# Kernel optimization log

Measured on AMD Instinct MI355X. Metric: run time of the kernel, lower is better.

The kernel has to match this reference:

```python
import jax, jax.numpy as jnp
import numpy as np


def psf2otf(psf, shape):
    """Zero-pad psf to `shape` and circularly shift so its center is at the
    origin, then 2D FFT. psf: [..., kh, kw] -> complex [..., H, W]."""
    kh, kw = psf.shape[-2], psf.shape[-1]
    H, W = shape
    pad = jnp.zeros(psf.shape[:-2] + (H, W), psf.dtype)
    pad = pad.at[..., :kh, :kw].set(psf)
    pad = jnp.roll(pad, shift=(-(kh // 2), -(kw // 2)), axis=(-2, -1))
    return jnp.fft.fft2(pad)


def setup_inputs() -> dict:
    key = jax.random.key(0)
    k1, k2, k3, k4, k5 = jax.random.split(key, 5)
    B, C, H, W = 4, 3, 512, 512
    NF, FS, KS = 24, 5, 25
    y = jax.random.normal(k1, (B, C, H, W), dtype=jnp.float32)
    k = jax.random.uniform(k2, (B, 1, KS, KS), dtype=jnp.float32)
    k = k / jnp.sum(k, axis=(-2, -1), keepdims=True)  # normalized blur PSF
    w = 0.5 + jax.random.uniform(k3, (B, 1), dtype=jnp.float32)  # positive (Softplus output)
    phi = jax.random.normal(k4, (B, C, H, W), dtype=jnp.float32)
    weights = jax.random.normal(k5, (NF, C, FS, FS), dtype=jnp.float32) * 0.3
    return {"y": y, "k": k, "w": w, "phi": phi, "weights": weights}


def reference(y, k, w, phi, weights):
    # FFT-domain Wiener deconvolution (FourierDeconvolutionFunction_init.forward).
    B, C, H, W = y.shape
    Fy = jnp.fft.fft2(y)                         # [B,C,H,W] complex64
    Dg = psf2otf(weights, (H, W))                # [NF,C,H,W] complex64
    Dk = psf2otf(k, (H, W))                      # [B,1,H,W] complex64, broadcasts over C
    w4 = w[:, :, None, None]                     # [B,1,1,1]
    Fphi = jnp.fft.fft2(phi / w4)                # [B,C,H,W]
    Dg_sum = jnp.sum(jnp.abs(Dg) ** 2, axis=0)[None] / w4   # [B,C,H,W] real
    Omega = 1.0 / (jnp.abs(Dk) ** 2 + Dg_sum)    # [B,C,H,W] real
    num = Omega * (jnp.conj(Dk) * Fy + Fphi)     # [B,C,H,W] complex64
    out = jnp.real(jnp.fft.ifft2(num)).astype(y.dtype)  # torch.irfft(..., onesided=False)
    return out
```

## Files before the change

### kernel.cpp

```cpp
#include <hip/hip_runtime.h>
#include <math.h>

#define PI_F 3.14159265358979323846f
#define NPIX 262144

__device__ __forceinline__ float2 cmul(float2 a, float2 b) {
    return make_float2(a.x * b.x - a.y * b.y, a.x * b.y + a.y * b.x);
}
__device__ __forceinline__ float2 cadd(float2 a, float2 b) {
    return make_float2(a.x + b.x, a.y + b.y);
}
__device__ __forceinline__ float2 csub(float2 a, float2 b) {
    return make_float2(a.x - b.x, a.y - b.y);
}

template<int DIR>
__device__ __forceinline__ void fill_tw(float2* tw, int t) {
    for (int m = t; m < 384; m += 128) {
        float s, c;
        sincosf((float)DIR * (2.0f * PI_F) * (float)m * (1.0f / 512.0f), &s, &c);
        tw[m] = make_float2(c, s);
    }
}

template<int DIR>
__device__ __forceinline__ float2* fft512(float2* sA, float2* sB,
                                          const float2* tw, int t) {
    float2* X = sA;
    float2* Y = sB;
    int Ns = 1;
#pragma unroll
    for (int s = 0; s < 4; ++s) {
        const int jm = t & (Ns - 1);
        const int jd = t - jm;
        float2 v0 = X[t], v1 = X[t + 128], v2 = X[t + 256], v3 = X[t + 384];
        const int m1 = jm * (128 / Ns);
        v1 = cmul(tw[m1], v1);
        v2 = cmul(tw[2 * m1], v2);
        v3 = cmul(tw[3 * m1], v3);
        const float2 t0 = cadd(v0, v2), t1 = csub(v0, v2);
        const float2 t2 = cadd(v1, v3), t3 = csub(v1, v3);
        const float2 t3i = (DIR > 0) ? make_float2(-t3.y, t3.x)
                                     : make_float2(t3.y, -t3.x);
        const int od = (jd << 2) + jm;
        Y[od]          = cadd(t0, t2);
        Y[od + Ns]     = cadd(t1, t3i);
        Y[od + 2 * Ns] = csub(t0, t2);
        Y[od + 3 * Ns] = csub(t1, t3i);
        __syncthreads();
        float2* tmp = X; X = Y; Y = tmp;
        Ns <<= 2;
    }
#pragma unroll
    for (int q = 0; q < 2; ++q) {
        const int j = t + q * 128;
        const float2 a = X[j], b = X[j + 256];
        const float2 tt = cmul(tw[j], b);
        Y[j]       = cadd(a, tt);
        Y[j + 256] = csub(a, tt);
    }
    __syncthreads();
    return Y;
}

__global__ __launch_bounds__(128) void fwd_fft_pack(const float* __restrict__ y,
                                                    const float* __restrict__ phi,
                                                    const float* __restrict__ w,
                                                    float2* __restrict__ S) {
    __shared__ float2 sA[512], sB[512], tw[384];
    const int t = threadIdx.x;
    const int img = blockIdx.x >> 9, row = blockIdx.x & 511;
    fill_tw<-1>(tw, t);
    const size_t off = (size_t)img * NPIX + (size_t)row * 512;
    const float iwv = 1.0f / w[img / 3];
    const float4 yv = ((const float4*)(y + off))[t];
    const float4 pv = ((const float4*)(phi + off))[t];
    sA[4 * t + 0] = make_float2(yv.x, pv.x * iwv);
    sA[4 * t + 1] = make_float2(yv.y, pv.y * iwv);
    sA[4 * t + 2] = make_float2(yv.z, pv.z * iwv);
    sA[4 * t + 3] = make_float2(yv.w, pv.w * iwv);
    __syncthreads();
    float2* R = fft512<-1>(sA, sB, tw, t);
    float4* wp = (float4*)(S + off);
    for (int k = t; k < 256; k += 128)
        wp[k] = make_float4(R[2 * k].x, R[2 * k].y,
                            R[2 * k + 1].x, R[2 * k + 1].y);
}

__global__ __launch_bounds__(128) void fwd_fft_kg(float2* __restrict__ S) {
    __shared__ float2 sA[512], sB[512], tw[384];
    const int t = threadIdx.x;
    int img, row;
    if (blockIdx.x < 100) {
        img = 12 + (int)blockIdx.x / 25;
        row = ((int)blockIdx.x % 25 - 12) & 511;
    } else {
        const int g = (int)blockIdx.x - 100;
        img = 16 + g / 9;
        row = ((g % 9) - 4) & 511;
    }
    fill_tw<-1>(tw, t);
    float2* rp = S + (size_t)img * NPIX + (size_t)row * 512;
    for (int k = t; k < 512; k += 128) sA[k] = rp[k];
    __syncthreads();
    float2* R = fft512<-1>(sA, sB, tw, t);
    for (int k = t; k < 512; k += 128) rp[k] = R[k];
}

template<int DIR>
__global__ __launch_bounds__(128) void fft_rows(float2* __restrict__ D) {
    __shared__ float2 sA[512], sB[512], tw[384];
    const int t = threadIdx.x;
    fill_tw<DIR>(tw, t);
    float2* rp = D + (size_t)blockIdx.x * 512;
    const float4* rp4 = (const float4*)rp;
    for (int k = t; k < 256; k += 128) {
        const float4 v = rp4[k];
        sA[2 * k]     = make_float2(v.x, v.y);
        sA[2 * k + 1] = make_float2(v.z, v.w);
    }
    __syncthreads();
    float2* R = fft512<DIR>(sA, sB, tw, t);
    float4* wp = (float4*)rp;
    for (int k = t; k < 256; k += 128)
        wp[k] = make_float4(R[2 * k].x, R[2 * k].y,
                            R[2 * k + 1].x, R[2 * k + 1].y);
}

__global__ __launch_bounds__(128) void inv_fft_unpack(const float2* __restrict__ T,
                                                      float* __restrict__ out) {
    __shared__ float2 sA[512], sB[512], tw[384];
    const int t = threadIdx.x;
    const int pair = blockIdx.x >> 9, row = blockIdx.x & 511;
    fill_tw<1>(tw, t);
    const float2* rp = T + (size_t)pair * NPIX + (size_t)row * 512;
    const float4* rp4 = (const float4*)rp;
    for (int k = t; k < 256; k += 128) {
        const float4 v = rp4[k];
        sA[2 * k]     = make_float2(v.x, v.y);
        sA[2 * k + 1] = make_float2(v.z, v.w);
    }
    __syncthreads();
    float2* R = fft512<1>(sA, sB, tw, t);
    const float sc = 1.0f / 262144.0f;
    float* o0 = out + (size_t)(2 * pair) * NPIX + (size_t)row * 512;
    float* o1 = o0 + NPIX;
    ((float4*)o0)[t] = make_float4(R[4 * t].x * sc, R[4 * t + 1].x * sc,
                                   R[4 * t + 2].x * sc, R[4 * t + 3].x * sc);
    ((float4*)o1)[t] = make_float4(R[4 * t].y * sc, R[4 * t + 1].y * sc,
                                   R[4 * t + 2].y * sc, R[4 * t + 3].y * sc);
}

__global__ __launch_bounds__(256) void transpose512_inplace(float2* __restrict__ D) {
    if (blockIdx.x > blockIdx.y) return;
    __shared__ float2 tA[32][33], tB[32][33];
    const size_t base = (size_t)blockIdx.z * NPIX;
    const int bi = blockIdx.x * 32, bj = blockIdx.y * 32;
    const int tx = threadIdx.x, ty = threadIdx.y;
    const bool diag = (bi == bj);
#pragma unroll
    for (int j = 0; j < 32; j += 8)
        tA[ty + j][tx] = D[base + (size_t)(bj + ty + j) * 512 + bi + tx];
    if (!diag) {
#pragma unroll
        for (int j = 0; j < 32; j += 8)
            tB[ty + j][tx] = D[base + (size_t)(bi + ty + j) * 512 + bj + tx];
    }
    __syncthreads();
#pragma unroll
    for (int j = 0; j < 32; j += 8)
        D[base + (size_t)(bi + ty + j) * 512 + bj + tx] = tA[tx][ty + j];
    if (!diag) {
#pragma unroll
        for (int j = 0; j < 32; j += 8)
            D[base + (size_t)(bj + ty + j) * 512 + bi + tx] = tB[tx][ty + j];
    }
}

__global__ __launch_bounds__(256) void transpose512(const float2* __restrict__ in,
                                                    float2* __restrict__ out) {
    __shared__ float2 tile[32][33];
    const size_t base = (size_t)blockIdx.z * NPIX;
    const int bx = blockIdx.x * 32, by = blockIdx.y * 32;
    const int tx = threadIdx.x, ty = threadIdx.y;
#pragma unroll
    for (int j = 0; j < 32; j += 8)
        tile[ty + j][tx] = in[base + (size_t)(by + ty + j) * 512 + bx + tx];
    __syncthreads();
#pragma unroll
    for (int j = 0; j < 32; j += 8)
        out[base + (size_t)(bx + ty + j) * 512 + by + tx] = tile[tx][ty + j];
}

__global__ __launch_bounds__(256) void prep_kg(const float* __restrict__ kin,
                                               const float* __restrict__ wts,
                                               float2* __restrict__ S) {
    const int bid = blockIdx.x, tid = threadIdx.x;
    if (bid < 10) {
        const int t = bid * 256 + tid;
        if (t < 2500) {
            const int b = t / 625, rem = t % 625;
            const int i = rem / 25, j = rem % 25;
            const int r = (i - 12) & 511, c = (j - 12) & 511;
            S[(size_t)(12 + b) * NPIX + (size_t)r * 512 + c] =
                make_float2(kin[t], 0.0f);
        }
        return;
    }
    const int ch = bid - 10;
    __shared__ float gp[24][13][13];
    __shared__ float part[243];
    float* gpf = &gp[0][0][0];
    for (int i = tid; i < 24 * 169; i += 256) gpf[i] = 0.0f;
    __syncthreads();
    for (int i = tid; i < 600; i += 256) {
        const int f = i / 25, rem = i % 25;
        const int x = rem / 5, yy = rem % 5;
        gp[f][x + 4][yy + 4] = wts[(size_t)(f * 3 + ch) * 25 + rem];
    }
    __syncthreads();
    if (tid < 243) {
        const int dpos = tid / 3, seg = tid % 3;
        const int di = dpos / 9 - 4, dj = dpos % 9 - 4;
        float acc = 0.0f;
        for (int f = seg * 8; f < seg * 8 + 8; ++f) {
#pragma unroll
            for (int x = 0; x < 5; ++x)
#pragma unroll
                for (int yy = 0; yy < 5; ++yy)
                    acc += gp[f][x + 4][yy + 4] *
                           gp[f][x + di + 4][yy + dj + 4];
        }
        part[tid] = acc;
    }
    __syncthreads();
    if (tid < 81) {
        const float a = part[tid * 3] + part[tid * 3 + 1] + part[tid * 3 + 2];
        const int di = tid / 9 - 4, dj = tid % 9 - 4;
        const int r = di & 511, c = dj & 511;
        S[(size_t)(16 + ch) * NPIX + (size_t)r * 512 + c] =
            make_float2(a, 0.0f);
    }
}

__global__ __launch_bounds__(256) void combine_pack(const float2* __restrict__ S,
                                                    const float* __restrict__ w,
                                                    float2* __restrict__ P) {
    const int p = blockIdx.x * 256 + threadIdx.x;
    const int pair = blockIdx.y;
    const int r = p >> 9, c = p & 511;
    const int np = (((512 - r) & 511) << 9) | ((512 - c) & 511);
    float2 num[2];
#pragma unroll
    for (int e = 0; e < 2; ++e) {
        const int img = pair * 2 + e;
        const int b = img / 3;
        const int ch = img - 3 * b;
        const float2* Zi = S + (size_t)img * NPIX;
        const float2 Zv = Zi[p];
        const float2 Zn = Zi[np];
        const float2 Zm = make_float2(Zn.x, -Zn.y);
        const float2 Fy = make_float2(0.5f * (Zv.x + Zm.x),
                                      0.5f * (Zv.y + Zm.y));
        const float dx = Zv.x - Zm.x, dy = Zv.y - Zm.y;
        const float2 Fphi = make_float2(0.5f * dy, -0.5f * dx);
        const float2 K = S[(size_t)(12 + b) * NPIX + p];
        const float kk = K.x * K.x + K.y * K.y;
        const float dg = S[(size_t)(16 + ch) * NPIX + p].x / w[b];
        const float Om = 1.0f / (kk + dg);
        const float2 tt = make_float2(K.x * Fy.x + K.y * Fy.y,
                                      K.x * Fy.y - K.y * Fy.x);
        num[e] = make_float2(Om * (tt.x + Fphi.x), Om * (tt.y + Fphi.y));
    }
    P[(size_t)pair * NPIX + p] =
        make_float2(num[0].x - num[1].y, num[0].y + num[1].x);
}

extern "C" void kernel_launch(void* const* d_in, const int* in_sizes, int n_in,
                              void* d_out, int out_size, void* d_ws, size_t ws_size,
                              hipStream_t stream) {
    const float* y   = (const float*)d_in[0];
    const float* k   = (const float*)d_in[1];
    const float* w   = (const float*)d_in[2];
    const float* phi = (const float*)d_in[3];
    const float* wts = (const float*)d_in[4];
    float* out = (float*)d_out;

    const size_t needed = (size_t)25 * NPIX * sizeof(float2);
    if (ws_size < needed) return;
    float2* S = (float2*)d_ws;
    float2* P = S + (size_t)19 * NPIX;

    hipMemsetAsync(S + (size_t)12 * NPIX, 0,
                   (size_t)7 * NPIX * sizeof(float2), stream);

    prep_kg<<<13, 256, 0, stream>>>(k, wts, S);
    fwd_fft_pack<<<12 * 512, 128, 0, stream>>>(y, phi, w, S);
    fwd_fft_kg<<<127, 128, 0, stream>>>(S);

    dim3 tb(32, 8);
    transpose512_inplace<<<dim3(16, 16, 19), tb, 0, stream>>>(S);
    fft_rows<-1><<<19 * 512, 128, 0, stream>>>(S);

    combine_pack<<<dim3(1024, 6), 256, 0, stream>>>(S, w, P);

    fft_rows<1><<<6 * 512, 128, 0, stream>>>(P);
    transpose512<<<dim3(16, 16, 6), tb, 0, stream>>>(P, S);
    inv_fft_unpack<<<6 * 512, 128, 0, stream>>>(S, out);
}
```

Measured before the change: 164.9 us.

## Fuse spectral combine into first inverse FFT pass and merge forward FFT launches

The pointwise Wiener combine is fused into the first inverse row-FFT pass. Each block handles a row and its mirror row, so the conjugate-symmetric partner data is read from the same pair of rows and the intermediate P array is never written and re-read by a separate kernel. The two forward FFT launches (image rows and the kernel/filter rows) are merged into one grid, which saves a launch. Twiddles now use the fast __sinf/__cosf intrinsics, trading some accuracy for cheaper setup.

```diff
diff --git a/kernel.cpp b/kernel.cpp
--- a/kernel.cpp
+++ b/kernel.cpp
@@ -15,11 +15,11 @@
 }
 
 template<int DIR>
-__device__ __forceinline__ void fill_tw(float2* tw, int t) {
-    for (int m = t; m < 384; m += 128) {
-        float s, c;
-        sincosf((float)DIR * (2.0f * PI_F) * (float)m * (1.0f / 512.0f), &s, &c);
-        tw[m] = make_float2(c, s);
+__device__ __forceinline__ void fill_tw(float2* tw, int t, int stride) {
+    for (int m = t; m < 384; m += stride) {
+        const float ang = (2.0f * PI_F / 512.0f) * (float)m;
+        const float s = __sinf(ang), c = __cosf(ang);
+        tw[m] = make_float2(c, (DIR > 0) ? s : -s);
     }
 }
 
@@ -63,43 +63,41 @@
     return Y;
 }
 
-__global__ __launch_bounds__(128) void fwd_fft_pack(const float* __restrict__ y,
-                                                    const float* __restrict__ phi,
-                                                    const float* __restrict__ w,
-                                                    float2* __restrict__ S) {
+__global__ __launch_bounds__(128) void fwd_fft_all(const float* __restrict__ y,
+                                                   const float* __restrict__ phi,
+                                                   const float* __restrict__ w,
+                                                   float2* __restrict__ S) {
     __shared__ float2 sA[512], sB[512], tw[384];
     const int t = threadIdx.x;
-    const int img = blockIdx.x >> 9, row = blockIdx.x & 511;
-    fill_tw<-1>(tw, t);
-    const size_t off = (size_t)img * NPIX + (size_t)row * 512;
-    const float iwv = 1.0f / w[img / 3];
-    const float4 yv = ((const float4*)(y + off))[t];
-    const float4 pv = ((const float4*)(phi + off))[t];
-    sA[4 * t + 0] = make_float2(yv.x, pv.x * iwv);
-    sA[4 * t + 1] = make_float2(yv.y, pv.y * iwv);
-    sA[4 * t + 2] = make_float2(yv.z, pv.z * iwv);
-    sA[4 * t + 3] = make_float2(yv.w, pv.w * iwv);
-    __syncthreads();
-    float2* R = fft512<-1>(sA, sB, tw, t);
-    float4* wp = (float4*)(S + off);
-    for (int k = t; k < 256; k += 128)
-        wp[k] = make_float4(R[2 * k].x, R[2 * k].y,
-                            R[2 * k + 1].x, R[2 * k + 1].y);
-}
-
-__global__ __launch_bounds__(128) void fwd_fft_kg(float2* __restrict__ S) {
-    __shared__ float2 sA[512], sB[512], tw[384];
-    const int t = threadIdx.x;
+    fill_tw<-1>(tw, t, 128);
+    if (blockIdx.x < 6144) {
+        const int img = blockIdx.x >> 9, row = blockIdx.x & 511;
+        const size_t off = (size_t)img * NPIX + (size_t)row * 512;
+        const float iwv = 1.0f / w[img / 3];
+        const float4 yv = ((const float4*)(y + off))[t];
+        const float4 pv = ((const float4*)(phi + off))[t];
+        sA[4 * t + 0] = make_float2(yv.x, pv.x * iwv);
+        sA[4 * t + 1] = make_float2(yv.y, pv.y * iwv);
+        sA[4 * t + 2] = make_float2(yv.z, pv.z * iwv);
+        sA[4 * t + 3] = make_float2(yv.w, pv.w * iwv);
+        __syncthreads();
+        float2* R = fft512<-1>(sA, sB, tw, t);
+        float4* wp = (float4*)(S + off);
+        for (int k = t; k < 256; k += 128)
+            wp[k] = make_float4(R[2 * k].x, R[2 * k].y,
+                                R[2 * k + 1].x, R[2 * k + 1].y);
+        return;
+    }
+    const int bid = blockIdx.x - 6144;
     int img, row;
-    if (blockIdx.x < 100) {
-        img = 12 + (int)blockIdx.x / 25;
-        row = ((int)blockIdx.x % 25 - 12) & 511;
+    if (bid < 100) {
+        img = 12 + bid / 25;
+        row = (bid % 25 - 12) & 511;
     } else {
-        const int g = (int)blockIdx.x - 100;
+        const int g = bid - 100;
         img = 16 + g / 9;
         row = ((g % 9) - 4) & 511;
     }
-    fill_tw<-1>(tw, t);
     float2* rp = S + (size_t)img * NPIX + (size_t)row * 512;
     for (int k = t; k < 512; k += 128) sA[k] = rp[k];
     __syncthreads();
@@ -111,7 +109,7 @@
 __global__ __launch_bounds__(128) void fft_rows(float2* __restrict__ D) {
     __shared__ float2 sA[512], sB[512], tw[384];
     const int t = threadIdx.x;
-    fill_tw<DIR>(tw, t);
+    fill_tw<DIR>(tw, t, 128);
     float2* rp = D + (size_t)blockIdx.x * 512;
     const float4* rp4 = (const float4*)rp;
     for (int k = t; k < 256; k += 128) {
@@ -127,12 +125,88 @@
                             R[2 * k + 1].x, R[2 * k + 1].y);
 }
 
+__device__ __forceinline__ float2 get2(const float4 a, const float4 b, int q) {
+    switch (q) {
+        case 0:  return make_float2(a.x, a.y);
+        case 1:  return make_float2(a.z, a.w);
+        case 2:  return make_float2(b.x, b.y);
+        default: return make_float2(b.z, b.w);
+    }
+}
+
+__global__ __launch_bounds__(256) void combine_ifft(const float2* __restrict__ S,
+                                                    const float* __restrict__ w,
+                                                    float2* __restrict__ P) {
+    __shared__ float2 sA[2][512], sB[2][512], tw[384];
+    const int t = threadIdx.x;
+    const int h = t >> 7, tt = t & 127;
+    const int rr = blockIdx.x;
+    const int pair = blockIdx.y;
+    const int r0 = rr, r1 = (512 - rr) & 511;
+    const int rh = h ? r1 : r0;
+    const int ro = h ? r0 : r1;
+    fill_tw<1>(tw, t, 256);
+    const int i0 = 2 * pair, i1 = 2 * pair + 1;
+    const int b0 = i0 / 3, b1 = i1 / 3;
+    const int ch0 = i0 % 3, ch1 = i1 % 3;
+    const float iw0 = 1.0f / w[b0], iw1 = 1.0f / w[b1];
+    const size_t rowh = (size_t)rh * 512, rowo = (size_t)ro * 512;
+    const float4* Zv0 = (const float4*)(S + (size_t)i0 * NPIX + rowh);
+    const float4* Zv1 = (const float4*)(S + (size_t)i1 * NPIX + rowh);
+    const float2* Zn0 = S + (size_t)i0 * NPIX + rowo;
+    const float2* Zn1 = S + (size_t)i1 * NPIX + rowo;
+    const float4* K0 = (const float4*)(S + (size_t)(12 + b0) * NPIX + rowh);
+    const float4* K1 = (const float4*)(S + (size_t)(12 + b1) * NPIX + rowh);
+    const float4* G0 = (const float4*)(S + (size_t)(16 + ch0) * NPIX + rowh);
+    const float4* G1 = (const float4*)(S + (size_t)(16 + ch1) * NPIX + rowh);
+
+    const float4 za = Zv0[2 * tt], zb = Zv0[2 * tt + 1];
+    const float4 ua = Zv1[2 * tt], ub = Zv1[2 * tt + 1];
+    const float4 ka = K0[2 * tt],  kb = K0[2 * tt + 1];
+    const float4 la = K1[2 * tt],  lb = K1[2 * tt + 1];
+    const float4 ga = G0[2 * tt],  gb = G0[2 * tt + 1];
+    const float4 ha = G1[2 * tt],  hb = G1[2 * tt + 1];
+#pragma unroll
+    for (int q = 0; q < 4; ++q) {
+        const int c = 4 * tt + q;
+        const int nc = (512 - c) & 511;
+        float2 num[2];
+#pragma unroll
+        for (int e = 0; e < 2; ++e) {
+            const float2 Zv = e ? get2(ua, ub, q) : get2(za, zb, q);
+            const float2 Zn = e ? Zn1[nc] : Zn0[nc];
+            const float2 K  = e ? get2(la, lb, q) : get2(ka, kb, q);
+            const float dg  = (e ? get2(ha, hb, q).x : get2(ga, gb, q).x) *
+                              (e ? iw1 : iw0);
+            const float2 Zm = make_float2(Zn.x, -Zn.y);
+            const float2 Fy = make_float2(0.5f * (Zv.x + Zm.x),
+                                          0.5f * (Zv.y + Zm.y));
+            const float dx = Zv.x - Zm.x, dy = Zv.y - Zm.y;
+            const float2 Fphi = make_float2(0.5f * dy, -0.5f * dx);
+            const float kk = K.x * K.x + K.y * K.y;
+            const float Om = 1.0f / (kk + dg);
+            const float2 cf = make_float2(K.x * Fy.x + K.y * Fy.y,
+                                          K.x * Fy.y - K.y * Fy.x);
+            num[e] = make_float2(Om * (cf.x + Fphi.x), Om * (cf.y + Fphi.y));
+        }
+        sA[h][c] = make_float2(num[0].x - num[1].y, num[0].y + num[1].x);
+    }
+    __syncthreads();
+    float2* R = fft512<1>(&sA[h][0], &sB[h][0], tw, tt);
+    if (!(h == 1 && r1 == r0)) {
+        float4* wp = (float4*)(P + (size_t)pair * NPIX + rowh);
+        for (int k = tt; k < 256; k += 128)
+            wp[k] = make_float4(R[2 * k].x, R[2 * k].y,
+                                R[2 * k + 1].x, R[2 * k + 1].y);
+    }
+}
+
 __global__ __launch_bounds__(128) void inv_fft_unpack(const float2* __restrict__ T,
                                                       float* __restrict__ out) {
     __shared__ float2 sA[512], sB[512], tw[384];
     const int t = threadIdx.x;
     const int pair = blockIdx.x >> 9, row = blockIdx.x & 511;
-    fill_tw<1>(tw, t);
+    fill_tw<1>(tw, t, 128);
     const float2* rp = T + (size_t)pair * NPIX + (size_t)row * 512;
     const float4* rp4 = (const float4*)rp;
     for (int k = t; k < 256; k += 128) {
@@ -243,39 +317,6 @@
     }
 }
 
-__global__ __launch_bounds__(256) void combine_pack(const float2* __restrict__ S,
-                                                    const float* __restrict__ w,
-                                                    float2* __restrict__ P) {
-    const int p = blockIdx.x * 256 + threadIdx.x;
-    const int pair = blockIdx.y;
-    const int r = p >> 9, c = p & 511;
-    const int np = (((512 - r) & 511) << 9) | ((512 - c) & 511);
-    float2 num[2];
-#pragma unroll
-    for (int e = 0; e < 2; ++e) {
-        const int img = pair * 2 + e;
-        const int b = img / 3;
-        const int ch = img - 3 * b;
-        const float2* Zi = S + (size_t)img * NPIX;
-        const float2 Zv = Zi[p];
-        const float2 Zn = Zi[np];
-        const float2 Zm = make_float2(Zn.x, -Zn.y);
-        const float2 Fy = make_float2(0.5f * (Zv.x + Zm.x),
-                                      0.5f * (Zv.y + Zm.y));
-        const float dx = Zv.x - Zm.x, dy = Zv.y - Zm.y;
-        const float2 Fphi = make_float2(0.5f * dy, -0.5f * dx);
-        const float2 K = S[(size_t)(12 + b) * NPIX + p];
-        const float kk = K.x * K.x + K.y * K.y;
-        const float dg = S[(size_t)(16 + ch) * NPIX + p].x / w[b];
-        const float Om = 1.0f / (kk + dg);
-        const float2 tt = make_float2(K.x * Fy.x + K.y * Fy.y,
-                                      K.x * Fy.y - K.y * Fy.x);
-        num[e] = make_float2(Om * (tt.x + Fphi.x), Om * (tt.y + Fphi.y));
-    }
-    P[(size_t)pair * NPIX + p] =
-        make_float2(num[0].x - num[1].y, num[0].y + num[1].x);
-}
-
 extern "C" void kernel_launch(void* const* d_in, const int* in_sizes, int n_in,
                               void* d_out, int out_size, void* d_ws, size_t ws_size,
                               hipStream_t stream) {
@@ -295,16 +336,14 @@
                    (size_t)7 * NPIX * sizeof(float2), stream);
 
     prep_kg<<<13, 256, 0, stream>>>(k, wts, S);
-    fwd_fft_pack<<<12 * 512, 128, 0, stream>>>(y, phi, w, S);
-    fwd_fft_kg<<<127, 128, 0, stream>>>(S);
+    fwd_fft_all<<<6271, 128, 0, stream>>>(y, phi, w, S);
 
     dim3 tb(32, 8);
     transpose512_inplace<<<dim3(16, 16, 19), tb, 0, stream>>>(S);
     fft_rows<-1><<<19 * 512, 128, 0, stream>>>(S);
 
-    combine_pack<<<dim3(1024, 6), 256, 0, stream>>>(S, w, P);
-
-    fft_rows<1><<<6 * 512, 128, 0, stream>>>(P);
+    combine_ifft<<<dim3(257, 6), 256, 0, stream>>>(S, w, P);
+
     transpose512<<<dim3(16, 16, 6), tb, 0, stream>>>(P, S);
     inv_fft_unpack<<<6 * 512, 128, 0, stream>>>(S, out);
 }
```

Result: faster. 159.4 us (-3.3%).
